# Kernel tuning notes

Hardware: AMD Instinct MI355X
Metric: run time of the kernel (lower is better)

## Reference

```python
import jax, jax.numpy as jnp
import numpy as np

B, S, H = 2, 2048, 2048
DK = DV = 128
HK, HV = 16, 32
G = HV // HK          # num_v_groups = 2
K = 4                 # conv kernel size
EPS = 1e-6
FQKVZ = 2 * HK * DK + 2 * HV * DV   # 12288
FBA = 2 * HV                        # 64
C = 2 * HK * DK + HV * DV           # conv channels = 8192


def setup_inputs() -> dict:
    key = jax.random.key(0)
    ks = jax.random.split(key, 10)
    f32 = jnp.float32
    return {
        "x": jax.random.normal(ks[0], (B, S, H), f32),
        "w_qkvz": jax.random.normal(ks[1], (H, FQKVZ), f32) * 0.02,
        "w_ba": jax.random.normal(ks[2], (H, FBA), f32) * 0.02,
        "conv_w": jax.random.normal(ks[3], (C, K), f32) * 0.1,
        "conv_b": jax.random.normal(ks[4], (C,), f32) * 0.02,
        "a_log": jax.random.normal(ks[5], (HV,), f32) * 0.5,
        "dt_bias": jax.random.normal(ks[6], (HV,), f32) * 0.5,
        "norm_w": jnp.ones((DV,), f32),
        "w_o": jax.random.normal(ks[7], (HV * DV, H), f32) * 0.02,
    }


def _l2norm(t):
    return t * jax.lax.rsqrt(jnp.sum(t * t, axis=-1, keepdims=True) + EPS)


def reference(x, w_qkvz, w_ba, conv_w, conv_b, a_log, dt_bias, norm_w, w_o):
    # fused input projections
    qkvz = x @ w_qkvz                                   # [B,S,FQKVZ]
    ba = x @ w_ba                                       # [B,S,FBA]

    # split_fused_inputs: per k-head layout [q(DK), k(DK), v(G*DV), z(G*DV)]
    qkvz = qkvz.reshape(B, S, HK, 2 * DK + 2 * G * DV)
    q = qkvz[..., :DK]                                  # [B,S,HK,DK]
    k = qkvz[..., DK:2 * DK]
    v = qkvz[..., 2 * DK:2 * DK + G * DV].reshape(B, S, HV, DV)
    z = qkvz[..., 2 * DK + G * DV:].reshape(B, S, HV, DV)
    ba = ba.reshape(B, S, HK, 2 * G)
    b = ba[..., :G].reshape(B, S, HV)
    a = ba[..., G:].reshape(B, S, HV)

    # causal depthwise conv1d + silu over concat(q,k,v) channels
    mixed = jnp.concatenate(
        [q.reshape(B, S, HK * DK), k.reshape(B, S, HK * DK), v.reshape(B, S, HV * DV)],
        axis=-1).transpose(0, 2, 1)                     # [B,C,S]
    mixed = jnp.pad(mixed, ((0, 0), (0, 0), (K - 1, 0)))
    mixed = jax.lax.conv_general_dilated(
        mixed, conv_w[:, None, :], (1,), 'VALID',
        dimension_numbers=('NCH', 'OIH', 'NCH'), feature_group_count=C)
    mixed = jax.nn.silu(mixed + conv_b[None, :, None]).transpose(0, 2, 1)  # [B,S,C]

    kd = HK * DK
    q = mixed[..., :kd].reshape(B, S, HK, DK)
    k = mixed[..., kd:2 * kd].reshape(B, S, HK, DK)
    v = mixed[..., 2 * kd:].reshape(B, S, HV, DV)

    # gating params
    g = -jnp.exp(a_log) * jax.nn.softplus(a + dt_bias)  # [B,S,HV]
    beta = jax.nn.sigmoid(b)                            # [B,S,HV]

    # GQA expand + qk l2-norm (kernel applies l2norm inside)
    q = jnp.repeat(q, G, axis=2)                        # [B,S,HV,DK]
    k = jnp.repeat(k, G, axis=2)
    q = _l2norm(q) * (DK ** -0.5)
    k = _l2norm(k)

    # gated delta-rule recurrence: S_t = exp(g_t) S_{t-1} + k_t (beta_t (v_t - k_t^T S))
    def step(Sm, inp):
        q_t, k_t, v_t, g_t, b_t = inp                   # [B,HV,*]
        Sm = Sm * jnp.exp(g_t)[..., None, None]
        kS = jnp.einsum('bhk,bhkv->bhv', k_t, Sm)
        dv = b_t[..., None] * (v_t - kS)
        Sm = Sm + k_t[..., None] * dv[:, :, None, :]
        o_t = jnp.einsum('bhk,bhkv->bhv', q_t, Sm)
        return Sm, o_t

    S0 = jnp.zeros((B, HV, DK, DV), q.dtype)
    seq = (jnp.moveaxis(q, 1, 0), jnp.moveaxis(k, 1, 0), jnp.moveaxis(v, 1, 0),
           jnp.moveaxis(g, 1, 0), jnp.moveaxis(beta, 1, 0))
    _, o = jax.lax.scan(step, S0, seq)                  # o: [S,B,HV,DV]
    o = jnp.moveaxis(o, 0, 1)                           # [B,S,HV,DV]

    # gated RMSNorm (Mamba-style: gate before norm)
    y = o * jax.nn.silu(z)
    var = jnp.mean(y * y, axis=-1, keepdims=True)
    y = y * jax.lax.rsqrt(var + EPS) * norm_w

    return y.reshape(B, S, HV * DV) @ w_o               # [B,S,H]
```

## Files before the change

### kernel.cpp

```cpp
#include <hip/hip_runtime.h>

typedef _Float16 f16;
typedef _Float16 f16x2 __attribute__((ext_vector_type(2)));
typedef _Float16 f16x4 __attribute__((ext_vector_type(4)));
typedef _Float16 f16x8 __attribute__((ext_vector_type(8)));
typedef float f32x4 __attribute__((ext_vector_type(4)));

#define QSCALE 0.08838834764831845f

#define RAW_BARRIER() do { \
    asm volatile("s_waitcnt lgkmcnt(0)" ::: "memory"); \
    __builtin_amdgcn_s_barrier(); \
    __builtin_amdgcn_sched_barrier(0); \
} while (0)

__global__ __launch_bounds__(256) void cvt16_kernel(const float* __restrict__ in,
                                                    f16* __restrict__ out, int n4) {
    int i = blockIdx.x * 256 + threadIdx.x;
    if (i >= n4) return;
    f32x4 v = ((const f32x4*)in)[i];
    f16x4 h;
    h[0] = (f16)v[0]; h[1] = (f16)v[1]; h[2] = (f16)v[2]; h[3] = (f16)v[3];
    ((f16x4*)out)[i] = h;
}

__global__ __launch_bounds__(256) void transpose16_kernel(const float* __restrict__ in,
                                                          f16* __restrict__ out, int R, int C) {
    __shared__ f16 tile[64][66];
    int c0 = blockIdx.x * 64, r0 = blockIdx.y * 64;
    int tid = threadIdx.x;
#pragma unroll
    for (int i = 0; i < 16; ++i) {
        int idx = i * 256 + tid;
        int r = idx >> 6, c = idx & 63;
        tile[r][c] = (f16)in[(long)(r0 + r) * C + (c0 + c)];
    }
    __syncthreads();
#pragma unroll
    for (int i = 0; i < 16; ++i) {
        int idx = i * 256 + tid;
        int orow = idx >> 6, oc = idx & 63;
        out[(long)(c0 + orow) * R + (r0 + oc)] = tile[oc][orow];
    }
}

template <int NJ, int F16OUT>
__global__ __launch_bounds__(512, 1) void gemm256_kernel(const f16* __restrict__ A,
                                                         const f16* __restrict__ Bt,
                                                         void* __restrict__ Cout,
                                                         int M, int N, int Kd) {
    constexpr int BN = 64 * NJ;
    constexpr int BNW = 16 * NJ;
    __shared__ f16 sA[2][256 * 64];
    __shared__ f16 sB[2][BN * 64];
    const int tid = threadIdx.x;
    const int lane = tid & 63, wv = tid >> 6;
    const int wm = wv >> 2, wn = wv & 3;
    const int m0 = blockIdx.y * 256, n0 = blockIdx.x * BN;
    const int lrow = lane & 15, lk = lane >> 4;
    const int nK = Kd >> 6;

    f32x4 acc[8][NJ] = {};
    f32x4 ra[4], rb[NJ];

    auto issue = [&](int k0) {
#pragma unroll
        for (int j = 0; j < 4; ++j) {
            int P = (tid + j * 512) * 16;
            int row = P >> 7;
            int koff = (P & 127) >> 1;
            ra[j] = *(const f32x4*)(A + (long)(m0 + row) * Kd + k0 + koff);
        }
#pragma unroll
        for (int j = 0; j < NJ; ++j) {
            int P = (tid + j * 512) * 16;
            int row = P >> 7;
            int koff = (P & 127) >> 1;
            rb[j] = *(const f32x4*)(Bt + (long)(n0 + row) * Kd + k0 + koff);
        }
    };
    auto commit = [&](int buf) {
#pragma unroll
        for (int j = 0; j < 4; ++j) {
            int P = (tid + j * 512) * 16;
            int row = P >> 7;
            int sw = P ^ ((row & 7) << 4);
            *(f32x4*)((char*)&sA[buf][0] + sw) = ra[j];
        }
#pragma unroll
        for (int j = 0; j < NJ; ++j) {
            int P = (tid + j * 512) * 16;
            int row = P >> 7;
            int sw = P ^ ((row & 7) << 4);
            *(f32x4*)((char*)&sB[buf][0] + sw) = rb[j];
        }
    };

    issue(0);
    commit(0);
    if (nK > 1) issue(64);
    RAW_BARRIER();

    int cur = 0;
    for (int t = 0; t < nK; ++t) {
        const char* bA = (const char*)&sA[cur][0];
        const char* bB = (const char*)&sB[cur][0];
        __builtin_amdgcn_s_setprio(1);
#pragma unroll
        for (int kk = 0; kk < 2; ++kk) {
            f16x8 bf[NJ];
#pragma unroll
            for (int j = 0; j < NJ; ++j) {
                int brow = wn * BNW + j * 16 + lrow;
                int bbyte = brow * 128 + kk * 64 + lk * 16;
                bf[j] = *(const f16x8*)(bB + (bbyte ^ ((brow & 7) << 4)));
            }
#pragma unroll
            for (int i = 0; i < 8; ++i) {
                int arow = wm * 128 + i * 16 + lrow;
                int abyte = arow * 128 + kk * 64 + lk * 16;
                f16x8 af = *(const f16x8*)(bA + (abyte ^ ((arow & 7) << 4)));
#pragma unroll
                for (int j = 0; j < NJ; ++j)
                    acc[i][j] = __builtin_amdgcn_mfma_f32_16x16x32_f16(af, bf[j], acc[i][j], 0, 0, 0);
            }
        }
        __builtin_amdgcn_s_setprio(0);
        if (t + 1 < nK) commit(cur ^ 1);
        if (t + 2 < nK) issue((t + 2) * 64);
        RAW_BARRIER();
        cur ^= 1;
    }

#pragma unroll
    for (int i = 0; i < 8; ++i) {
        int gm_base = m0 + wm * 128 + i * 16 + lk * 4;
#pragma unroll
        for (int j = 0; j < NJ; ++j) {
            int gn = n0 + wn * BNW + j * 16 + lrow;
#pragma unroll
            for (int r = 0; r < 4; ++r) {
                long idx = (long)(gm_base + r) * N + gn;
                if (F16OUT) ((f16*)Cout)[idx] = (f16)acc[i][j][r];
                else        ((float*)Cout)[idx] = acc[i][j][r];
            }
        }
    }
}

__global__ __launch_bounds__(256) void ba_gemm_kernel(const float* __restrict__ x,
                                                      const float* __restrict__ w,
                                                      const float* __restrict__ a_log,
                                                      const float* __restrict__ dt_bias,
                                                      float* __restrict__ gout,
                                                      float* __restrict__ bt) {
    __shared__ float xs[4][2048];
    int tid = threadIdx.x;
    int t0 = blockIdx.x * 4;
    int o = tid & 63, tg = tid >> 6;
    for (int i = tid; i < 4 * 512; i += 256) {
        int tok = i >> 9, kq = i & 511;
        ((f32x4*)&xs[tok][0])[kq] = ((const f32x4*)(x + (long)(t0 + tok) * 2048))[kq];
    }
    __syncthreads();
    const float* xr = &xs[tg][0];
    float acc = 0.f;
    for (int k = 0; k < 2048; ++k)
        acc = fmaf(xr[k], w[(long)k * 64 + o], acc);

    int hv = ((o >> 2) << 1) | (o & 1);
    bool isB = (o & 2) == 0;
    int tok = t0 + tg;
    int b = tok >> 11, s = tok & 2047;
    long oidx = ((long)b * 32 + hv) * 2048 + s;
    if (isB) {
        bt[oidx] = 1.f / (1.f + expf(-acc));
    } else {
        float xx = acc + dt_bias[hv];
        float sp = (xx > 20.f) ? xx : log1pf(expf(xx));
        gout[oidx] = -expf(a_log[hv]) * sp;
    }
}

__global__ __launch_bounds__(256) void conv_kernel(const f16* __restrict__ qkvz,
                                                   const float* __restrict__ cw,
                                                   const float* __restrict__ cb,
                                                   f16* __restrict__ qh,
                                                   f16* __restrict__ kh,
                                                   f16* __restrict__ vh,
                                                   f16* __restrict__ khT) {
    __shared__ float Lin[35 * 128];
    __shared__ float Lout[32 * 128];
    __shared__ float Lsc[32];
    int g = blockIdx.x;
    int s0 = blockIdx.y * 32;
    int b = blockIdx.z;
    int tid = threadIdx.x;
    int colbase, chbase;
    f16* outp;
    bool donorm;
    bool isk = false;
    int hk = 0;
    float nmul;
    if (g < 16) {
        colbase = g * 768; chbase = g * 128;
        outp = qh + (((long)b * 16 + g) * 2048 + s0) * 128;
        donorm = true; nmul = QSCALE;
    } else if (g < 32) {
        hk = g - 16;
        colbase = hk * 768 + 128; chbase = 2048 + hk * 128;
        outp = kh + (((long)b * 16 + hk) * 2048 + s0) * 128;
        donorm = true; nmul = 1.f; isk = true;
    } else {
        int hv = g - 32;
        colbase = (hv >> 1) * 768 + 256 + (hv & 1) * 128; chbase = 4096 + hv * 128;
        outp = vh + (((long)b * 32 + hv) * 2048 + s0) * 128;
        donorm = false; nmul = 1.f;
    }
    for (int ci = tid; ci < 35 * 16; ci += 256) {
        int sr = ci >> 4, cc = (ci & 15) * 8;
        int s = s0 + sr - 3;
        f32x4 lo = {}, hi = {};
        if (s >= 0) {
            f16x8 v = *(const f16x8*)(qkvz + ((long)b * 2048 + s) * 12288 + colbase + cc);
#pragma unroll
            for (int e = 0; e < 4; ++e) { lo[e] = (float)v[e]; hi[e] = (float)v[4 + e]; }
        }
        *(f32x4*)&Lin[sr * 128 + cc] = lo;
        *(f32x4*)&Lin[sr * 128 + cc + 4] = hi;
    }
    __syncthreads();
    int c = tid & 127, sg = tid >> 7;
    float w0 = cw[(chbase + c) * 4 + 0];
    float w1 = cw[(chbase + c) * 4 + 1];
    float w2 = cw[(chbase + c) * 4 + 2];
    float w3 = cw[(chbase + c) * 4 + 3];
    float bias = cb[chbase + c];
#pragma unroll
    for (int j = 0; j < 16; ++j) {
        int sl = sg * 16 + j;
        float v = w0 * Lin[sl * 128 + c] + w1 * Lin[(sl + 1) * 128 + c] +
                  w2 * Lin[(sl + 2) * 128 + c] + w3 * Lin[(sl + 3) * 128 + c] + bias;
        v = v / (1.f + expf(-v));
        Lout[sl * 128 + c] = v;
    }
    __syncthreads();
    if (donorm) {
        int token = tid >> 3, part = tid & 7;
        float ss = 0.f;
#pragma unroll
        for (int i = 0; i < 16; ++i) {
            float v = Lout[token * 128 + part * 16 + i];
            ss += v * v;
        }
        ss += __shfl_xor(ss, 1); ss += __shfl_xor(ss, 2); ss += __shfl_xor(ss, 4);
        if (part == 0) Lsc[token] = rsqrtf(ss + 1e-6f) * nmul;
        __syncthreads();
#pragma unroll
        for (int j = 0; j < 16; ++j) {
            int sl = sg * 16 + j;
            outp[(long)sl * 128 + c] = (f16)(Lout[sl * 128 + c] * Lsc[sl]);
        }
        if (isk) {
            int dk = tid >> 1, sh = tid & 1;
            f16x8 v0, v1;
#pragma unroll
            for (int i = 0; i < 8; ++i) {
                v0[i] = (f16)(Lout[(sh * 16 + i) * 128 + dk] * Lsc[sh * 16 + i]);
                v1[i] = (f16)(Lout[(sh * 16 + 8 + i) * 128 + dk] * Lsc[sh * 16 + 8 + i]);
            }
            f16* kt = khT + ((long)(b * 16 + hk) * 128 + dk) * 2048 + s0 + sh * 16;
            *(f16x8*)kt = v0;
            *(f16x8*)(kt + 8) = v1;
        }
    } else {
#pragma unroll
        for (int j = 0; j < 16; ++j) {
            int sl = sg * 16 + j;
            outp[(long)sl * 128 + c] = (f16)Lout[sl * 128 + c];
        }
    }
}

__global__ __launch_bounds__(64) void chunk_pre_kernel(const f16* __restrict__ qh,
                                                       const f16* __restrict__ kh,
                                                       const f16* __restrict__ vh,
                                                       const float* __restrict__ gb,
                                                       const float* __restrict__ bt,
                                                       f16* __restrict__ Wg,
                                                       f16* __restrict__ T2ng,
                                                       f16* __restrict__ d0g,
                                                       float* __restrict__ pvg) {
    __shared__ f16 VTl[128 * 32];
    __shared__ float KKl[32 * 32];
    __shared__ float RL[32 * 32];
    __shared__ float Tf[32 * 33];
    __shared__ f16 Tl[32 * 64];
    __shared__ float cuml[32], bl[32], pl[32];

    int bid = blockIdx.x;
    int chunk = bid & 63;
    int hv = (bid >> 6) & 31;
    int b = bid >> 11;
    int bh = b * 16 + (hv >> 1);
    int l = threadIdx.x;
    int h = l >> 4, c = l & 15;
    long chid = bid;

    const f16* kbase = kh + ((long)bh * 2048 + chunk * 32) * 128;
    const f16* qbase = qh + ((long)bh * 2048 + chunk * 32) * 128;
    const f16* vbase = vh + (((long)b * 32 + hv) * 2048 + chunk * 32) * 128;
    const float* gp = gb + ((long)b * 32 + hv) * 2048 + chunk * 32;
    const float* bp = bt + ((long)b * 32 + hv) * 2048 + chunk * 32;

    f16x8 fk[2][4], fq[2][4];
#pragma unroll
    for (int ti = 0; ti < 2; ++ti)
#pragma unroll
        for (int kk = 0; kk < 4; ++kk) {
            fk[ti][kk] = *(const f16x8*)(kbase + (c + 16 * ti) * 128 + kk * 32 + h * 8);
            fq[ti][kk] = *(const f16x8*)(qbase + (c + 16 * ti) * 128 + kk * 32 + h * 8);
        }

    float gv = (l < 32) ? gp[l] : 0.f;
#pragma unroll
    for (int d = 1; d < 32; d <<= 1) {
        float t2 = __shfl_up(gv, d);
        if (l >= d) gv += t2;
    }
    if (l < 32) { cuml[l] = gv; bl[l] = bp[l]; pl[l] = expf(gv); }
    __syncthreads();

#pragma unroll
    for (int it = 0; it < 8; ++it) {
        int idx = (l + it * 64) * 8;
        int row = idx >> 7, col = idx & 127;
        f16x8 v = *(const f16x8*)(vbase + (long)row * 128 + col);
        float be = bl[row];
#pragma unroll
        for (int e = 0; e < 8; ++e) {
            int dv = col + e;
            int byte = (dv * 64 + row * 2) ^ ((dv & 3) << 4);
            *(f16*)((char*)VTl + byte) = (f16)((float)v[e] * be);
        }
    }
#pragma unroll
    for (int it = 0; it < 16; ++it) {
        int e = l * 16 + it;
        int i = e >> 5, j = e & 31;
        RL[e] = (j <= i) ? expf(cuml[i] - cuml[j]) : 0.f;
    }
    __syncthreads();

    {
        f32x4 acc[2][2] = {};
#pragma unroll
        for (int kk = 0; kk < 4; ++kk) {
            acc[0][0] = __builtin_amdgcn_mfma_f32_16x16x32_f16(fk[0][kk], fk[0][kk], acc[0][0], 0, 0, 0);
            acc[0][1] = __builtin_amdgcn_mfma_f32_16x16x32_f16(fk[0][kk], fk[1][kk], acc[0][1], 0, 0, 0);
            acc[1][0] = __builtin_amdgcn_mfma_f32_16x16x32_f16(fk[1][kk], fk[0][kk], acc[1][0], 0, 0, 0);
            acc[1][1] = __builtin_amdgcn_mfma_f32_16x16x32_f16(fk[1][kk], fk[1][kk], acc[1][1], 0, 0, 0);
        }
#pragma unroll
        for (int ti = 0; ti < 2; ++ti)
#pragma unroll
            for (int tj = 0; tj < 2; ++tj)
#pragma unroll
                for (int r = 0; r < 4; ++r)
                    KKl[(h * 4 + r + 16 * ti) * 32 + c + 16 * tj] = acc[ti][tj][r];
    }
    {
        f32x4 acc[2][2] = {};
#pragma unroll
        for (int kk = 0; kk < 4; ++kk) {
            acc[0][0] = __builtin_amdgcn_mfma_f32_16x16x32_f16(fq[0][kk], fk[0][kk], acc[0][0], 0, 0, 0);
            acc[0][1] = __builtin_amdgcn_mfma_f32_16x16x32_f16(fq[0][kk], fk[1][kk], acc[0][1], 0, 0, 0);
            acc[1][0] = __builtin_amdgcn_mfma_f32_16x16x32_f16(fq[1][kk], fk[0][kk], acc[1][0], 0, 0, 0);
            acc[1][1] = __builtin_amdgcn_mfma_f32_16x16x32_f16(fq[1][kk], fk[1][kk], acc[1][1], 0, 0, 0);
        }
        __syncthreads();
#pragma unroll
        for (int ti = 0; ti < 2; ++ti)
#pragma unroll
            for (int tj = 0; tj < 2; ++tj)
#pragma unroll
                for (int r = 0; r < 4; ++r) {
                    int i = h * 4 + r + 16 * ti, j = c + 16 * tj;
                    Wg[chid * 1024 + i * 32 + j] = (f16)(acc[ti][tj][r] * RL[i * 32 + j]);
                }
    }

    if (l < 32) {
        int j = l;
        for (int i = 0; i < 32; ++i) {
            float s = (i == j) ? 1.f : 0.f;
            float bi = bl[i];
            for (int ll = j; ll < i; ++ll)
                s -= bi * KKl[i * 32 + ll] * RL[i * 32 + ll] * Tf[ll * 33 + j];
            Tf[i * 33 + j] = s;
        }
        float bpj = bl[j] * pl[j];
        for (int i = 0; i < 32; ++i) {
            float tv = (i >= j) ? Tf[i * 33 + j] : 0.f;
            int byte = (i * 128 + j * 2) ^ ((i & 3) << 4);
            *(f16*)((char*)Tl + byte) = (f16)tv;
            T2ng[chid * 1024 + i * 32 + j] = (f16)(-tv * bpj);
        }
        pvg[chid * 64 + j] = pl[j];
        pvg[chid * 64 + 32 + j] = expf(cuml[31] - cuml[j]);
    }
    __syncthreads();

    {
        f16x8 fT[2];
#pragma unroll
        for (int ti = 0; ti < 2; ++ti) {
            int row = c + 16 * ti;
            fT[ti] = *(const f16x8*)((const char*)Tl + ((row * 128 + h * 16) ^ ((row & 3) << 4)));
        }
#pragma unroll
        for (int nj = 0; nj < 8; ++nj) {
            int dv = c + 16 * nj;
            f16x8 fv = *(const f16x8*)((const char*)VTl + ((dv * 64 + h * 16) ^ ((dv & 3) << 4)));
            f32x4 a0 = {}, a1 = {};
            a0 = __builtin_amdgcn_mfma_f32_16x16x32_f16(fT[0], fv, a0, 0, 0, 0);
            a1 = __builtin_amdgcn_mfma_f32_16x16x32_f16(fT[1], fv, a1, 0, 0, 0);
            f16x4 s0, s1;
#pragma unroll
            for (int r = 0; r < 4; ++r) { s0[r] = (f16)a0[r]; s1[r] = (f16)a1[r]; }
            *(f16x4*)(d0g + chid * 4096 + (long)dv * 32 + 4 * h) = s0;
            *(f16x4*)(d0g + chid * 4096 + (long)dv * 32 + 16 + 4 * h) = s1;
        }
    }
}

struct CR {
    f16x8 fk[2][4], fq[2][4], fkt[8], fT[2], fW[2];
    f16x4 fd0[2];
    f32x4 pva, pvb, kwa, kwb;
    float pc;
};

__global__ __launch_bounds__(64, 1) void scan_kernel(const f16* __restrict__ qh,
                                                     const f16* __restrict__ kh,
                                                     const f16* __restrict__ khT,
                                                     const f16* __restrict__ Wg,
                                                     const f16* __restrict__ T2ng,
                                                     const f16* __restrict__ d0g,
                                                     const float* __restrict__ pvg,
                                                     f16* __restrict__ ob) {
    __shared__ f16 Sl[2][16 * 128];
    __shared__ f16 AKl[16 * 32];
    __shared__ f16 Dl[16 * 32];

    int pbid = blockIdx.x;
    int bid = (pbid & 7) * 64 + (pbid >> 3);
    int vs = bid & 7;
    int hv = (bid >> 3) & 31;
    int b = bid >> 8;
    int bh32 = b * 32 + hv;
    int bh = b * 16 + (hv >> 1);
    int l = threadIdx.x, h = l >> 4, c = l & 15;

    const f16* kb = kh + (long)bh * 2048 * 128;
    const f16* qb = qh + (long)bh * 2048 * 128;
    const f16* ktb = khT + (long)bh * 128 * 2048;

    f16x8 z = {};
#pragma unroll
    for (int it = 0; it < 4; ++it) *(f16x8*)((char*)Sl[0] + (l + it * 64) * 16) = z;

    int cur = 0;

    auto loadC = [&](CR& R, int ch) {
        long chid = (long)bh32 * 64 + ch;
#pragma unroll
        for (int ti = 0; ti < 2; ++ti) {
            long row = (long)ch * 32 + c + 16 * ti;
#pragma unroll
            for (int kk = 0; kk < 4; ++kk) {
                R.fk[ti][kk] = *(const f16x8*)(kb + row * 128 + kk * 32 + h * 8);
                R.fq[ti][kk] = *(const f16x8*)(qb + row * 128 + kk * 32 + h * 8);
            }
            R.fT[ti] = *(const f16x8*)(T2ng + chid * 1024 + (c + 16 * ti) * 32 + h * 8);
            R.fW[ti] = *(const f16x8*)(Wg + chid * 1024 + (c + 16 * ti) * 32 + h * 8);
        }
#pragma unroll
        for (int ti = 0; ti < 8; ++ti)
            R.fkt[ti] = *(const f16x8*)(ktb + (long)(c + 16 * ti) * 2048 + ch * 32 + h * 8);
#pragma unroll
        for (int ti = 0; ti < 2; ++ti)
            R.fd0[ti] = *(const f16x4*)(d0g + chid * 4096 +
                                        (long)(vs * 16 + c) * 32 + 16 * ti + 4 * h);
        R.pva = *(const f32x4*)(pvg + chid * 64 + 4 * h);
        R.pvb = *(const f32x4*)(pvg + chid * 64 + 16 + 4 * h);
        R.pc = pvg[chid * 64 + 31];
        R.kwa = *(const f32x4*)(pvg + chid * 64 + 32 + h * 8);
        R.kwb = *(const f32x4*)(pvg + chid * 64 + 36 + h * 8);
    };

    auto computeC = [&](const CR& R, int ch) {
        const int dv = c;
        f16x8 fS[4];
#pragma unroll
        for (int kk = 0; kk < 4; ++kk)
            fS[kk] = *(const f16x8*)((char*)Sl[cur] +
                                     (dv * 256 + ((kk * 64 + h * 16) ^ ((dv & 7) << 4))));
        f32x4 AK[2] = {}, AQ[2] = {};
#pragma unroll
        for (int ti = 0; ti < 2; ++ti)
#pragma unroll
            for (int kk = 0; kk < 4; ++kk) {
                AK[ti] = __builtin_amdgcn_mfma_f32_16x16x32_f16(R.fk[ti][kk], fS[kk], AK[ti], 0, 0, 0);
                AQ[ti] = __builtin_amdgcn_mfma_f32_16x16x32_f16(R.fq[ti][kk], fS[kk], AQ[ti], 0, 0, 0);
            }
#pragma unroll
        for (int ti = 0; ti < 2; ++ti) {
            f16x4 t;
#pragma unroll
            for (int r = 0; r < 4; ++r) t[r] = (f16)AK[ti][r];
            *(f16x4*)((char*)AKl + ((dv * 64 + 32 * ti + 8 * h) ^ ((dv & 3) << 4))) = t;
        }
        f32x4 Dv[2];
#pragma unroll
        for (int ti = 0; ti < 2; ++ti)
#pragma unroll
            for (int r = 0; r < 4; ++r) Dv[ti][r] = (float)R.fd0[ti][r];
        {
            f16x8 fak = *(const f16x8*)((char*)AKl + ((dv * 64 + h * 16) ^ ((dv & 3) << 4)));
#pragma unroll
            for (int ti = 0; ti < 2; ++ti)
                Dv[ti] = __builtin_amdgcn_mfma_f32_16x16x32_f16(R.fT[ti], fak, Dv[ti], 0, 0, 0);
        }
#pragma unroll
        for (int ti = 0; ti < 2; ++ti) {
            f16x4 t;
#pragma unroll
            for (int r = 0; r < 4; ++r) t[r] = (f16)Dv[ti][r];
            *(f16x4*)((char*)Dl + ((dv * 64 + 32 * ti + 8 * h) ^ ((dv & 3) << 4))) = t;
        }
        f16x8 fdl = *(const f16x8*)((char*)Dl + ((dv * 64 + h * 16) ^ ((dv & 3) << 4)));
        f32x4 Ov[2];
#pragma unroll
        for (int ti = 0; ti < 2; ++ti)
#pragma unroll
            for (int r = 0; r < 4; ++r)
                Ov[ti][r] = AQ[ti][r] * (ti ? R.pvb[r] : R.pva[r]);
#pragma unroll
        for (int ti = 0; ti < 2; ++ti)
            Ov[ti] = __builtin_amdgcn_mfma_f32_16x16x32_f16(R.fW[ti], fdl, Ov[ti], 0, 0, 0);
#pragma unroll
        for (int ti = 0; ti < 2; ++ti)
#pragma unroll
            for (int r = 0; r < 4; ++r) {
                long tok = (long)b * 2048 + ch * 32 + 16 * ti + 4 * h + r;
                ob[tok * 4096 + hv * 128 + vs * 16 + c] = (f16)Ov[ti][r];
            }
#pragma unroll
        for (int ti = 0; ti < 8; ++ti) {
            f16x8 fa;
#pragma unroll
            for (int e = 0; e < 8; ++e)
                fa[e] = (f16)((float)R.fkt[ti][e] * (e < 4 ? R.kwa[e] : R.kwb[e - 4]));
            int sbyte = (dv * 256 + (32 * ti + 8 * h)) ^ ((dv & 7) << 4);
            f16x4 sold = *(const f16x4*)((char*)Sl[cur] + sbyte);
            f32x4 acc;
#pragma unroll
            for (int r = 0; r < 4; ++r) acc[r] = R.pc * (float)sold[r];
            acc = __builtin_amdgcn_mfma_f32_16x16x32_f16(fa, fdl, acc, 0, 0, 0);
            f16x4 snew;
#pragma unroll
            for (int r = 0; r < 4; ++r) snew[r] = (f16)acc[r];
            *(f16x4*)((char*)Sl[cur ^ 1] + sbyte) = snew;
        }
        cur ^= 1;
        RAW_BARRIER();
    };

    CR A, B;
    loadC(A, 0);
    RAW_BARRIER();
    for (int ch = 0; ch < 64; ch += 2) {
        loadC(B, ch + 1);
        computeC(A, ch);
        loadC(A, ch + 2 < 64 ? ch + 2 : 63);
        computeC(B, ch + 1);
    }
}

__global__ __launch_bounds__(256) void gate_kernel(const f16* __restrict__ o,
                                                   const f16* __restrict__ qkvz,
                                                   const float* __restrict__ norm_w,
                                                   f16* __restrict__ y) {
    int token = blockIdx.x;
    int tid = threadIdx.x;
    int hv = tid >> 3, part = tid & 7;
    int dv0 = part * 16;
    const f16* orow = o + ((long)token * 32 + hv) * 128 + dv0;
    long zcol = (long)(hv >> 1) * 768 + 512 + (hv & 1) * 128 + dv0;
    const f16* zrow = qkvz + (long)token * 12288 + zcol;
    f16x8 ov0 = *(const f16x8*)orow, ov1 = *(const f16x8*)(orow + 8);
    f16x8 zv0 = *(const f16x8*)zrow, zv1 = *(const f16x8*)(zrow + 8);
    float yv[16];
    float ss = 0.f;
#pragma unroll
    for (int i = 0; i < 16; ++i) {
        float ovf = (float)(i < 8 ? ov0[i] : ov1[i - 8]);
        float zvf = (float)(i < 8 ? zv0[i] : zv1[i - 8]);
        float gt = zvf / (1.f + expf(-zvf));
        float v = ovf * gt;
        yv[i] = v;
        ss += v * v;
    }
    ss += __shfl_xor(ss, 1); ss += __shfl_xor(ss, 2); ss += __shfl_xor(ss, 4);
    float scale = rsqrtf(ss * (1.f / 128.f) + 1e-6f);
    f16* yrow = y + (long)token * 4096 + hv * 128 + dv0;
    f16x8 y0, y1;
#pragma unroll
    for (int i = 0; i < 8; ++i) {
        y0[i] = (f16)(yv[i] * scale * norm_w[dv0 + i]);
        y1[i] = (f16)(yv[8 + i] * scale * norm_w[dv0 + 8 + i]);
    }
    *(f16x8*)yrow = y0;
    *(f16x8*)(yrow + 8) = y1;
}

extern "C" void kernel_launch(void* const* d_in, const int* in_sizes, int n_in,
                              void* d_out, int out_size, void* d_ws, size_t ws_size,
                              hipStream_t stream) {
    const float* x       = (const float*)d_in[0];
    const float* w_qkvz  = (const float*)d_in[1];
    const float* w_ba    = (const float*)d_in[2];
    const float* conv_w  = (const float*)d_in[3];
    const float* conv_b  = (const float*)d_in[4];
    const float* a_log   = (const float*)d_in[5];
    const float* dt_bias = (const float*)d_in[6];
    const float* norm_w  = (const float*)d_in[7];
    const float* w_o     = (const float*)d_in[8];
    float* out = (float*)d_out;

    char* ws = (char*)d_ws;
    const size_t MB = 1024 * 1024;
    f16*   qkvz16 = (f16*)ws;
    f16*   x16    = (f16*)(ws + 96 * MB);
    f16*   WT     = (f16*)(ws + 112 * MB);
    f16*   d0g    = (f16*)(ws + 96 * MB);
    f16*   Wg     = (f16*)(ws + 128 * MB);
    f16*   T2ng   = (f16*)(ws + 136 * MB);
    f16*   khT    = (f16*)(ws + 144 * MB);
    f16*   WTo    = (f16*)(ws + 160 * MB);
    f16*   qh     = (f16*)(ws + 176 * MB);
    f16*   kh     = (f16*)(ws + 192 * MB);
    f16*   vh     = (f16*)(ws + 208 * MB);
    f16*   ob     = (f16*)(ws + 208 * MB);
    f16*   y16    = (f16*)(ws + 176 * MB);
    float* gbuf   = (float*)(ws + 240 * MB);
    float* btb    = (float*)(ws + 240 * MB + 512 * 1024);
    float* pvg    = (float*)(ws + 241 * MB);

    cvt16_kernel<<<8192, 256, 0, stream>>>(x, x16, 4096 * 2048 / 4);
    transpose16_kernel<<<dim3(12288 / 64, 2048 / 64), 256, 0, stream>>>(w_qkvz, WT, 2048, 12288);
    transpose16_kernel<<<dim3(2048 / 64, 4096 / 64), 256, 0, stream>>>(w_o, WTo, 4096, 2048);

    gemm256_kernel<4, 1><<<dim3(12288 / 256, 4096 / 256), 512, 0, stream>>>(x16, WT, qkvz16, 4096, 12288, 2048);
    ba_gemm_kernel<<<1024, 256, 0, stream>>>(x, w_ba, a_log, dt_bias, gbuf, btb);

    conv_kernel<<<dim3(64, 64, 2), 256, 0, stream>>>(qkvz16, conv_w, conv_b, qh, kh, vh, khT);
    chunk_pre_kernel<<<4096, 64, 0, stream>>>(qh, kh, vh, gbuf, btb, Wg, T2ng, d0g, pvg);
    scan_kernel<<<512, 64, 0, stream>>>(qh, kh, khT, Wg, T2ng, d0g, pvg, ob);

    gate_kernel<<<4096, 256, 0, stream>>>(ob, qkvz16, norm_w, y16);

    gemm256_kernel<2, 0><<<dim3(2048 / 128, 4096 / 256), 512, 0, stream>>>(y16, WTo, out, 4096, 2048, 4096);
}
```

Measured before the change: 694.4 us.

## Interleave GEMM global loads and LDS commits across four MFMA phases

Splits each K-tile of the fp16 GEMM main loop into four phases. Each phase loads A/B fragments from LDS, commits one slice of the prefetched next tile into the other LDS buffer, issues one slice of the global load two tiles ahead, and then runs a quarter of the MFMAs. The goal is to spread global and LDS traffic across the MFMA work instead of bunching it after the compute, so memory latency overlaps with matrix math. In exchange it adds an extra barrier per phase and changes the register live ranges.

```diff
diff --git a/kernel.cpp b/kernel.cpp
--- a/kernel.cpp
+++ b/kernel.cpp
@@ -79,6 +79,20 @@
             rb[j] = *(const f32x4*)(Bt + (long)(n0 + row) * Kd + k0 + koff);
         }
     };
+    auto issue_slice = [&](int k0, int p) {
+        {
+            int P = (tid + p * 512) * 16;
+            int row = P >> 7;
+            int koff = (P & 127) >> 1;
+            ra[p] = *(const f32x4*)(A + (long)(m0 + row) * Kd + k0 + koff);
+        }
+        if (p < NJ) {
+            int P = (tid + p * 512) * 16;
+            int row = P >> 7;
+            int koff = (P & 127) >> 1;
+            rb[p] = *(const f32x4*)(Bt + (long)(n0 + row) * Kd + k0 + koff);
+        }
+    };
     auto commit = [&](int buf) {
 #pragma unroll
         for (int j = 0; j < 4; ++j) {
@@ -95,6 +109,20 @@
             *(f32x4*)((char*)&sB[buf][0] + sw) = rb[j];
         }
     };
+    auto commit_slice = [&](int buf, int p) {
+        {
+            int P = (tid + p * 512) * 16;
+            int row = P >> 7;
+            int sw = P ^ ((row & 7) << 4);
+            *(f32x4*)((char*)&sA[buf][0] + sw) = ra[p];
+        }
+        if (p < NJ) {
+            int P = (tid + p * 512) * 16;
+            int row = P >> 7;
+            int sw = P ^ ((row & 7) << 4);
+            *(f32x4*)((char*)&sB[buf][0] + sw) = rb[p];
+        }
+    };
 
     issue(0);
     commit(0);
@@ -105,29 +133,39 @@
     for (int t = 0; t < nK; ++t) {
         const char* bA = (const char*)&sA[cur][0];
         const char* bB = (const char*)&sB[cur][0];
-        __builtin_amdgcn_s_setprio(1);
-#pragma unroll
-        for (int kk = 0; kk < 2; ++kk) {
-            f16x8 bf[NJ];
-#pragma unroll
-            for (int j = 0; j < NJ; ++j) {
-                int brow = wn * BNW + j * 16 + lrow;
-                int bbyte = brow * 128 + kk * 64 + lk * 16;
-                bf[j] = *(const f16x8*)(bB + (bbyte ^ ((brow & 7) << 4)));
+        f16x8 bfk[NJ];
+#pragma unroll
+        for (int p = 0; p < 4; ++p) {
+            const int kk = p >> 1, ih = p & 1;
+            if (ih == 0) {
+#pragma unroll
+                for (int j = 0; j < NJ; ++j) {
+                    int brow = wn * BNW + j * 16 + lrow;
+                    int bbyte = brow * 128 + kk * 64 + lk * 16;
+                    bfk[j] = *(const f16x8*)(bB + (bbyte ^ ((brow & 7) << 4)));
+                }
             }
-#pragma unroll
-            for (int i = 0; i < 8; ++i) {
-                int arow = wm * 128 + i * 16 + lrow;
+            f16x8 af[4];
+#pragma unroll
+            for (int ii = 0; ii < 4; ++ii) {
+                int arow = wm * 128 + (ih * 4 + ii) * 16 + lrow;
                 int abyte = arow * 128 + kk * 64 + lk * 16;
-                f16x8 af = *(const f16x8*)(bA + (abyte ^ ((arow & 7) << 4)));
+                af[ii] = *(const f16x8*)(bA + (abyte ^ ((arow & 7) << 4)));
+            }
+            if (t + 1 < nK) commit_slice(cur ^ 1, p);
+            if (t + 2 < nK) issue_slice((t + 2) * 64, p);
+            __builtin_amdgcn_s_barrier();
+            asm volatile("s_waitcnt lgkmcnt(0)" ::: "memory");
+            __builtin_amdgcn_sched_barrier(0);
+            __builtin_amdgcn_s_setprio(1);
+#pragma unroll
+            for (int ii = 0; ii < 4; ++ii)
 #pragma unroll
                 for (int j = 0; j < NJ; ++j)
-                    acc[i][j] = __builtin_amdgcn_mfma_f32_16x16x32_f16(af, bf[j], acc[i][j], 0, 0, 0);
-            }
-        }
-        __builtin_amdgcn_s_setprio(0);
-        if (t + 1 < nK) commit(cur ^ 1);
-        if (t + 2 < nK) issue((t + 2) * 64);
+                    acc[ih * 4 + ii][j] =
+                        __builtin_amdgcn_mfma_f32_16x16x32_f16(af[ii], bfk[j], acc[ih * 4 + ii][j], 0, 0, 0);
+            __builtin_amdgcn_s_setprio(0);
+        }
         RAW_BARRIER();
         cur ^= 1;
     }
```

New measurement: 734.1 us. 5.7% more time.
